# Kernel tuning notes

Hardware: AMD Instinct MI355X
Metric: run time of the kernel (lower is better)

## Reference

```python
import jax, jax.numpy as jnp
import numpy as np

MAX_FPS = 30.0
NUM_HEADS = 8


def _rope(x, times):
    # x: [B, H, T, D] with D even; interleaved rotary (even/odd pairs)
    B, H, T, D = x.shape
    inv_freq = 1.0 / (10000.0 ** (jnp.arange(0, D, 2, dtype=jnp.float32) / D))  # [D/2]
    pos = jnp.round(times * MAX_FPS)                       # [B, T]
    freqs = pos[:, :, None] * inv_freq[None, None, :]      # [B, T, D/2]
    cos = jnp.cos(freqs)[:, None, :, :]                    # [B, 1, T, D/2]
    sin = jnp.sin(freqs)[:, None, :, :]
    xp = x.reshape(B, H, T, D // 2, 2)
    x0, x1 = xp[..., 0], xp[..., 1]                        # even-index, odd-index elems
    r0 = x0 * cos - x1 * sin
    r1 = x0 * sin + x1 * cos
    return jnp.stack([r0, r1], axis=-1).reshape(B, H, T, D)


def setup_inputs() -> dict:
    key = jax.random.key(0)
    k1, k2, k3, k4, k5 = jax.random.split(key, 5)
    B, N, C = 4, 2048, 512
    x = jax.random.normal(k1, (B, N, C), dtype=jnp.float32)
    mask = jnp.zeros((B, N), dtype=jnp.float32)  # additive mask, 0 = attend
    # times in seconds; rounded to frame indices inside RoPE
    times = jax.random.uniform(k2, (B, N), dtype=jnp.float32) * (N / MAX_FPS)
    bound_qkv = float(np.sqrt(6.0 / (C + 3 * C)))
    Wqkv = jax.random.uniform(k3, (3 * C, C), minval=-bound_qkv, maxval=bound_qkv, dtype=jnp.float32)
    bound_p = float(np.sqrt(6.0 / (C + C)))
    Wproj = jax.random.uniform(k4, (C, C), minval=-bound_p, maxval=bound_p, dtype=jnp.float32)
    bproj = jnp.zeros((C,), dtype=jnp.float32)
    return {"x": x, "mask": mask, "times": times, "Wqkv": Wqkv,
            "Wproj": Wproj, "bproj": bproj, "num_cls_token": 0}


def reference(x, mask, times, Wqkv, Wproj, bproj, num_cls_token):
    B, N, C = x.shape
    H = NUM_HEADS
    Dh = C // H
    qkv = (x @ Wqkv.T).reshape(B, N, 3, H, Dh).transpose(2, 0, 3, 1, 4)  # [3,B,H,N,Dh]
    q, k, v = qkv[0], qkv[1], qkv[2]
    if num_cls_token > 0:
        c_q, q = q[:, :, :num_cls_token], q[:, :, num_cls_token:]
        c_k, k = k[:, :, :num_cls_token], k[:, :, num_cls_token:]
        t = times
        q = _rope(q, t)
        k = _rope(k, t)
        q = jnp.concatenate([c_q, q], axis=2)
        k = jnp.concatenate([c_k, k], axis=2)
    else:
        q = _rope(q, times)
        k = _rope(k, times)
    scale = 1.0 / jnp.sqrt(jnp.float32(Dh))
    scores = jnp.einsum('bhqd,bhkd->bhqk', q, k) * scale + mask[:, None, None, :]
    attn = jax.nn.softmax(scores, axis=-1)
    out = jnp.einsum('bhqk,bhkd->bhqd', attn, v)           # [B,H,N,Dh]
    out = out.transpose(0, 2, 1, 3).reshape(B, N, C)
    return out @ Wproj.T + bproj
```

## Files before the change

### kernel.cpp

```cpp
#include <hip/hip_runtime.h>
#include <math.h>

#define BB 4
#define NN 2048
#define CC 512
#define HH 8
#define DH 64
#define MM (BB*NN)
#define QKV_N (3*CC)
#define NSP 2
#define SLICE ((size_t)32 * NN)

typedef _Float16 f16;
typedef __attribute__((ext_vector_type(2))) _Float16 f16x2;
typedef __attribute__((ext_vector_type(4))) _Float16 f16x4;
typedef __attribute__((ext_vector_type(8))) _Float16 f16x8;
typedef __attribute__((ext_vector_type(4))) float f32x4;
typedef __attribute__((ext_vector_type(2))) __fp16 h16x2;

#define L2E 1.4426950408889634f
#define QSCL (0.125f * L2E)

__device__ __forceinline__ float fast_exp2(float x) {
#if __has_builtin(__builtin_amdgcn_exp2f)
    return __builtin_amdgcn_exp2f(x);
#else
    float r;
    asm volatile("v_exp_f32 %0, %1\n\ts_nop 1" : "=v"(r) : "v"(x));
    return r;
#endif
}

__device__ __forceinline__ float fdot2(f16x2 a, f16x2 b, float c) {
#if __has_builtin(__builtin_amdgcn_fdot2)
    return __builtin_amdgcn_fdot2(a, b, c, false);
#else
    return c + (float)a[0]*(float)b[0] + (float)a[1]*(float)b[1];
#endif
}

#define GL16(g, l) __builtin_amdgcn_global_load_lds(                       \
    (const __attribute__((address_space(1))) void*)(g),                    \
    (__attribute__((address_space(3))) void*)(l), 16, 0, 0)

#define SX4 (MM*CC/4)
#define SW4 (QKV_N*CC/4)
#define SP4 (CC*CC/4)
#define CAST_T (SX4 + SW4 + SP4)
#define TAB_T (MM * 32)
#define WT_T  (MM / 8)
__global__ __launch_bounds__(256) void cast_tab_kernel(
    const float* __restrict__ x, const float* __restrict__ wqkv,
    const float* __restrict__ wproj, const float* __restrict__ times,
    const float* __restrict__ mask,
    f16* __restrict__ xh, f16* __restrict__ wqh, f16* __restrict__ wph,
    float2* __restrict__ tab, f16* __restrict__ wtab)
{
    const int t = blockIdx.x * 256 + threadIdx.x;
    if (t < CAST_T) {
        const float* src; f16* dst; int i;
        bool qscale = false;
        if (t < SX4)            { src = x;     dst = xh;  i = t; }
        else if (t < SX4 + SW4) { src = wqkv;  dst = wqh; i = t - SX4;
                                  qscale = (i < CC*CC/4); }
        else                    { src = wproj; dst = wph; i = t - SX4 - SW4; }
        f32x4 v = *(const f32x4*)(src + 4 * (size_t)i);
        if (qscale) v *= QSCL;
        f16x4 h = { (f16)v[0], (f16)v[1], (f16)v[2], (f16)v[3] };
        *(f16x4*)(dst + 4 * (size_t)i) = h;
    } else if (t < CAST_T + TAB_T) {
        const int idx = t - CAST_T;
        const int row = idx >> 5, fi = idx & 31;
        const float pos = rintf(times[row] * 30.0f);
        const float invf = exp2f((float)fi * (-13.287712379549449f / 32.0f));
        float s, c;
        sincosf(pos * invf, &s, &c);
        tab[idx] = make_float2(c, s);
    } else {
        const int i = t - CAST_T - TAB_T;
        f32x4 m0 = *(const f32x4*)(mask + 8 * (size_t)i);
        f32x4 m1 = *(const f32x4*)(mask + 8 * (size_t)i + 4);
        f16x8 wv;
        #pragma unroll
        for (int r = 0; r < 4; ++r) {
            wv[r]     = (f16)fast_exp2(m0[r] * L2E);
            wv[4 + r] = (f16)fast_exp2(m1[r] * L2E);
        }
        *(f16x8*)(wtab + 8 * (size_t)i) = wv;
    }
}

__global__ __launch_bounds__(256) void qkv_gemm(
    const f16* __restrict__ xh, const f16* __restrict__ wh,
    const float2* __restrict__ tab, const int* __restrict__ nclsp,
    const f16* __restrict__ wtab,
    f16* __restrict__ qo, f16* __restrict__ ksw, f16* __restrict__ vsw)
{
    __shared__ __align__(16) char smem[16896];
    f16 (*As)[32] = (f16 (*)[32])smem;
    f16 (*Bs)[32] = (f16 (*)[32])(smem + 8192);

    const int m0 = blockIdx.x * 128;
    const int n0 = blockIdx.y * 128;
    const int tid = threadIdx.x;
    const int lane = tid & 63;
    const int w = tid >> 6;
    const int wm = (w & 1) * 64, wn = (w >> 1) * 64;
    const int l15 = lane & 15, quad = lane >> 4;

    const int sr = tid >> 2;
    const int sc = (tid & 3) * 8;
    const f16* ga0 = xh + (size_t)(m0 + sr) * CC + sc;
    const f16* ga1 = xh + (size_t)(m0 + sr + 64) * CC + sc;
    const f16* gb0 = wh + (size_t)(n0 + sr) * CC + sc;
    const f16* gb1 = wh + (size_t)(n0 + sr + 64) * CC + sc;
    f16* la0 = &As[sr][sc];      f16* la1 = &As[sr + 64][sc];
    f16* lb0 = &Bs[sr][sc];      f16* lb1 = &Bs[sr + 64][sc];

    f32x4 acc[4][4] = {};
    for (int k0 = 0; k0 < CC; k0 += 32) {
        __syncthreads();
        GL16(ga0 + k0, la0);
        GL16(ga1 + k0, la1);
        GL16(gb0 + k0, lb0);
        GL16(gb1 + k0, lb1);
        __syncthreads();

        f16x8 af[4], bf[4];
        #pragma unroll
        for (int mi = 0; mi < 4; ++mi)
            af[mi] = *(const f16x8*)&As[wm + mi*16 + l15][quad * 8];
        #pragma unroll
        for (int ni = 0; ni < 4; ++ni)
            bf[ni] = *(const f16x8*)&Bs[wn + ni*16 + l15][quad * 8];
        #pragma unroll
        for (int mi = 0; mi < 4; ++mi)
            #pragma unroll
            for (int ni = 0; ni < 4; ++ni)
                acc[mi][ni] = __builtin_amdgcn_mfma_f32_16x16x32_f16(
                    af[mi], bf[ni], acc[mi][ni], 0, 0, 0);
    }
    __syncthreads();

    const int which = n0 >> 9;
    const int b     = m0 >> 11;
    const int mloc  = m0 & (NN - 1);
    const int hbase = (n0 & 511) >> 6;

    if (which < 2) {
        f16 (*Tr)[132] = (f16 (*)[132])smem;
        const int ncls = *nclsp;
        #pragma unroll
        for (int c = 0; c < 2; ++c) {
            if ((w & 1) == c) {
                #pragma unroll
                for (int mi = 0; mi < 4; ++mi)
                    #pragma unroll
                    for (int ni = 0; ni < 4; ++ni)
                        #pragma unroll
                        for (int r = 0; r < 4; ++r)
                            Tr[16*mi + quad*4 + r][wn + 16*ni + l15] =
                                (f16)acc[mi][ni][r];
            }
            __syncthreads();
            const int row = tid >> 2, cg = tid & 3;
            const int n   = mloc + c*64 + row;
            const int hh  = hbase + (cg >> 1);
            const int d0  = (cg & 1) * 32;
            f16x8 vv[4];
            #pragma unroll
            for (int j = 0; j < 4; ++j)
                vv[j] = *(const f16x8*)&Tr[row][cg*32 + j*8];
            if (n >= ncls) {
                const f32x4* t4 = (const f32x4*)(tab + ((size_t)b*NN + n)*32
                                                 + (d0 >> 1));
                #pragma unroll
                for (int j = 0; j < 4; ++j) {
                    f32x4 cs0 = t4[2*j];
                    f32x4 cs1 = t4[2*j + 1];
                    #pragma unroll
                    for (int p = 0; p < 4; ++p) {
                        const float co = (p < 2) ? cs0[(p & 1)*2]
                                                 : cs1[(p & 1)*2];
                        const float s  = (p < 2) ? cs0[(p & 1)*2 + 1]
                                                 : cs1[(p & 1)*2 + 1];
                        const float x0 = (float)vv[j][2*p];
                        const float x1 = (float)vv[j][2*p+1];
                        vv[j][2*p]   = (f16)(x0*co - x1*s);
                        vv[j][2*p+1] = (f16)(x0*s + x1*co);
                    }
                }
            }
            if (which == 0) {
                f16* qp = qo + (((size_t)(b*HH + hh))*NN + n)*DH + d0;
                #pragma unroll
                for (int j = 0; j < 4; ++j)
                    *(f16x8*)(qp + 8*j) = vv[j];
            } else {
                const int ktile = (mloc >> 6) + c;
                f16* kp = ksw + ((((size_t)(b*HH + hh))*32 + ktile)*64 + row)*64;
                #pragma unroll
                for (int j = 0; j < 4; ++j) {
                    const int blk = (d0 >> 3) + j;
                    *(f16x8*)(kp + ((blk ^ (row & 7)) * 8)) = vv[j];
                }
            }
            if (c == 0) __syncthreads();
        }
        return;
    }

    f16 (*Tv)[66] = (f16 (*)[66])smem;
    #pragma unroll
    for (int c = 0; c < 2; ++c) {
        if ((w & 1) == c) {
            #pragma unroll
            for (int mi = 0; mi < 4; ++mi)
                #pragma unroll
                for (int ni = 0; ni < 4; ++ni) {
                    f16x4 pk = { (f16)acc[mi][ni][0], (f16)acc[mi][ni][1],
                                 (f16)acc[mi][ni][2], (f16)acc[mi][ni][3] };
                    *(f16x4*)&Tv[wn + 16*ni + l15][16*mi + quad*4] = pk;
                }
        }
        __syncthreads();
        const int rr = tid >> 1;
        const int d  = rr & 63, hh = hbase + (rr >> 6);
        const int ktile = (mloc >> 6) + c;
        f16* vp = vsw + ((((size_t)(b*HH + hh))*32 + ktile)*64 + d)*64;
        #pragma unroll
        for (int j = 0; j < 4; ++j) {
            const int blk = (tid & 1)*4 + j;
            f16x8 t = *(const f16x8*)&Tv[rr][(tid & 1)*32 + j*8];
            t *= *(const f16x8*)&wtab[(size_t)b*NN + mloc + c*64
                                      + (tid & 1)*32 + j*8];
            *(f16x8*)(vp + ((blk ^ (d & 7)) * 8)) = t;
        }
        if (c == 0) __syncthreads();
    }
}

__global__ __launch_bounds__(256, 4) void attn_kernel(
    const f16* __restrict__ qg, const f16* __restrict__ ksw,
    const f16* __restrict__ vsw, const f16* __restrict__ wtab,
    f16* __restrict__ On, float* __restrict__ lbuf)
{
    __shared__ __align__(16) f16 asm_[4][4096];

    const int bh = blockIdx.x, qt = blockIdx.y, sp = blockIdx.z;
    const int b = bh >> 3;
    const int tid = threadIdx.x;
    const int w = tid >> 6, lane = tid & 63;
    const int l15 = lane & 15, quad = lane >> 4;
    const int rho = l15 & 7;

    const f16* qbase = qg + ((size_t)bh * NN + qt*128 + w*32) * DH;
    const f16* kt0 = ksw + ((size_t)bh * 32 + sp*16) * 4096;
    const f16* vt0 = vsw + ((size_t)bh * 32 + sp*16) * 4096;
    const f16* wsl = wtab + (size_t)b * NN + sp*1024;

    f16x8 Bq[2][2];
    #pragma unroll
    for (int ni = 0; ni < 2; ++ni)
        #pragma unroll
        for (int kc = 0; kc < 2; ++kc)
            Bq[ni][kc] = *(const f16x8*)(qbase + (size_t)(16*ni + l15) * DH
                                         + kc*32 + quad*8);

    const f32x4 fz = {};
    f32x4 O[2][4] = {};
    float accL[2] = {};

    {
        const f16* ks = kt0 + tid*8;
        const f16* vs = vt0 + tid*8;
        GL16(ks,        &asm_[0][tid*8]);
        GL16(ks + 2048, &asm_[0][2048 + tid*8]);
        GL16(vs,        &asm_[1][tid*8]);
        GL16(vs + 2048, &asm_[1][2048 + tid*8]);
    }

    for (int kt = 0; kt < 16; ++kt) {
        const int cur = (kt & 1) * 2;
        __syncthreads();
        if (kt + 1 < 16) {
            const int nxt = 2 - cur;
            const f16* ks = kt0 + (size_t)(kt+1)*4096 + tid*8;
            const f16* vs = vt0 + (size_t)(kt+1)*4096 + tid*8;
            GL16(ks,        &asm_[nxt][tid*8]);
            GL16(ks + 2048, &asm_[nxt][2048 + tid*8]);
            GL16(vs,        &asm_[nxt+1][tid*8]);
            GL16(vs + 2048, &asm_[nxt+1][2048 + tid*8]);
        }
        const f16 (*Kh)[64] = (const f16 (*)[64])asm_[cur];
        const f16 (*Vt)[64] = (const f16 (*)[64])asm_[cur + 1];

        f32x4 st[4][2];
        const int aw = (quad ^ rho) * 8;
        __builtin_amdgcn_s_setprio(1);
        #pragma unroll
        for (int mi = 0; mi < 4; ++mi) {
            f16x8 Ak0 = *(const f16x8*)&Kh[16*mi + l15][aw];
            f16x8 Ak1 = *(const f16x8*)&Kh[16*mi + l15][aw ^ 32];
            #pragma unroll
            for (int ni = 0; ni < 2; ++ni) {
                f32x4 t0 = __builtin_amdgcn_mfma_f32_16x16x32_f16(
                    Ak0, Bq[ni][0], fz, 0, 0, 0);
                st[mi][ni] = __builtin_amdgcn_mfma_f32_16x16x32_f16(
                    Ak1, Bq[ni][1], t0, 0, 0, 0);
            }
        }
        __builtin_amdgcn_s_setprio(0);

        f16x4 ph[4][2];
        #pragma unroll
        for (int mi = 0; mi < 4; ++mi) {
            #pragma unroll
            for (int ni = 0; ni < 2; ++ni) {
                float e0 = fast_exp2(st[mi][ni][0]);
                float e1 = fast_exp2(st[mi][ni][1]);
                float e2 = fast_exp2(st[mi][ni][2]);
                float e3 = fast_exp2(st[mi][ni][3]);
                h16x2 lo = __builtin_amdgcn_cvt_pkrtz(e0, e1);
                h16x2 hi = __builtin_amdgcn_cvt_pkrtz(e2, e3);
                f16x2 lo2 = __builtin_bit_cast(f16x2, lo);
                f16x2 hi2 = __builtin_bit_cast(f16x2, hi);
                ph[mi][ni] = __builtin_shufflevector(lo2, hi2, 0, 1, 2, 3);
            }
            f16x4 wv = *(const f16x4*)(wsl + kt*64 + 16*mi + quad*4);
            f16x2 wlo = __builtin_shufflevector(wv, wv, 0, 1);
            f16x2 whi = __builtin_shufflevector(wv, wv, 2, 3);
            #pragma unroll
            for (int ni = 0; ni < 2; ++ni) {
                f16x2 plo = __builtin_shufflevector(ph[mi][ni], ph[mi][ni], 0, 1);
                f16x2 phi = __builtin_shufflevector(ph[mi][ni], ph[mi][ni], 2, 3);
                accL[ni] = fdot2(plo, wlo, accL[ni]);
                accL[ni] = fdot2(phi, whi, accL[ni]);
            }
        }

        __builtin_amdgcn_s_setprio(1);
        #pragma unroll
        for (int g = 0; g < 2; ++g) {
            f16x8 p0 = __builtin_shufflevector(ph[2*g][0], ph[2*g+1][0],
                                               0, 1, 2, 3, 4, 5, 6, 7);
            f16x8 p1 = __builtin_shufflevector(ph[2*g][1], ph[2*g+1][1],
                                               0, 1, 2, 3, 4, 5, 6, 7);
            const int vb1 = (((4*g + (quad >> 1)) ^ rho) * 8) + (quad & 1) * 4;
            const int vb2 = (((4*g + 2 + (quad >> 1)) ^ rho) * 8) + (quad & 1) * 4;
            #pragma unroll
            for (int nd = 0; nd < 4; ++nd) {
                f16x4 av0 = *(const f16x4*)&Vt[16*nd + l15][vb1];
                f16x4 av1 = *(const f16x4*)&Vt[16*nd + l15][vb2];
                f16x8 Av = __builtin_shufflevector(av0, av1,
                                                   0, 1, 2, 3, 4, 5, 6, 7);
                O[0][nd] = __builtin_amdgcn_mfma_f32_16x16x32_f16(
                    Av, p0, O[0][nd], 0, 0, 0);
                O[1][nd] = __builtin_amdgcn_mfma_f32_16x16x32_f16(
                    Av, p1, O[1][nd], 0, 0, 0);
            }
        }
        __builtin_amdgcn_s_setprio(0);
    }

    #pragma unroll
    for (int ni = 0; ni < 2; ++ni) {
        float l = accL[ni];
        l += __shfl_xor(l, 16);
        l += __shfl_xor(l, 32);
        const float inv = 1.0f / l;
        const int qrow = qt*128 + w*32 + 16*ni + l15;
        const size_t rbase = (size_t)sp * SLICE + (size_t)bh * NN + qrow;
        f16* obase = On + rbase * DH;
        #pragma unroll
        for (int nd = 0; nd < 4; ++nd) {
            f32x4 o = O[ni][nd] * inv;
            f16x4 oh = { (f16)o[0], (f16)o[1], (f16)o[2], (f16)o[3] };
            *(f16x4*)(obase + 16*nd + quad*4) = oh;
        }
        if (quad == 0)
            lbuf[rbase] = l;
    }
}

__global__ __launch_bounds__(256) void proj_gemm(
    const f16* __restrict__ On, const float* __restrict__ lbuf,
    const f16* __restrict__ wh, const float* __restrict__ bias,
    float* __restrict__ out)
{
    __shared__ f16 As[128][32];
    __shared__ f16 Bs[64][32];
    const int m0 = blockIdx.x * 128;
    const int n0 = blockIdx.y * 64;
    const int tid = threadIdx.x;
    const int lane = tid & 63;
    const int w = tid >> 6;
    const int wm = (w & 1) * 64, wn = (w >> 1) * 32;
    const int l15 = lane & 15, quad = lane >> 4;

    const int b  = m0 >> 11;
    const int q0 = m0 & (NN - 1);

    const int sr = tid >> 2;
    const int sc = (tid & 3) * 8;
    const f16* gb0 = wh + (size_t)(n0 + sr) * CC + sc;
    f16* lb0 = &Bs[sr][sc];

    f32x4 acc[4][2] = {};
    for (int k0 = 0; k0 < CC; k0 += 32) {
        const int h  = k0 >> 6;
        const int d0 = k0 & 63;
        __syncthreads();
        GL16(gb0 + k0, lb0);
        const size_t row0 = (size_t)(b*HH + h) * NN + q0 + sr;
        #pragma unroll
        for (int rr = 0; rr < 2; ++rr) {
            const size_t row = row0 + rr*64;
            const float l0 = lbuf[row], l1 = lbuf[SLICE + row];
            const float inv = 1.0f / (l0 + l1);
            const float w0 = l0 * inv, w1 = l1 * inv;
            f16x8 a0 = *(const f16x8*)(On + row * DH + d0 + sc);
            f16x8 a1 = *(const f16x8*)(On + (SLICE + row) * DH + d0 + sc);
            f16x8 o;
            #pragma unroll
            for (int r = 0; r < 8; ++r)
                o[r] = (f16)(w0 * (float)a0[r] + w1 * (float)a1[r]);
            *(f16x8*)&As[sr + rr*64][sc] = o;
        }
        __syncthreads();

        f16x8 af[4], bf[2];
        #pragma unroll
        for (int mi = 0; mi < 4; ++mi)
            af[mi] = *(const f16x8*)&As[wm + mi*16 + l15][quad * 8];
        #pragma unroll
        for (int ni = 0; ni < 2; ++ni)
            bf[ni] = *(const f16x8*)&Bs[wn + ni*16 + l15][quad * 8];
        #pragma unroll
        for (int mi = 0; mi < 4; ++mi)
            #pragma unroll
            for (int ni = 0; ni < 2; ++ni)
                acc[mi][ni] = __builtin_amdgcn_mfma_f32_16x16x32_f16(
                    af[mi], bf[ni], acc[mi][ni], 0, 0, 0);
    }

    float bb[2];
    #pragma unroll
    for (int ni = 0; ni < 2; ++ni)
        bb[ni] = bias[n0 + wn + ni*16 + l15];

    #pragma unroll
    for (int mi = 0; mi < 4; ++mi)
        #pragma unroll
        for (int r = 0; r < 4; ++r) {
            const int m = m0 + wm + mi*16 + quad*4 + r;
            #pragma unroll
            for (int ni = 0; ni < 2; ++ni)
                out[(size_t)m * CC + n0 + wn + ni*16 + l15] = acc[mi][ni][r] + bb[ni];
        }
}

extern "C" void kernel_launch(void* const* d_in, const int* in_sizes, int n_in,
                              void* d_out, int out_size, void* d_ws, size_t ws_size,
                              hipStream_t stream)
{
    const float* x     = (const float*)d_in[0];
    const float* mask  = (const float*)d_in[1];
    const float* times = (const float*)d_in[2];
    const float* Wqkv  = (const float*)d_in[3];
    const float* Wproj = (const float*)d_in[4];
    const float* bproj = (const float*)d_in[5];
    const int*   ncls  = (const int*)d_in[6];
    float* out = (float*)d_out;

    const size_t per = (size_t)BB * HH * NN * DH;
    f16* xh  = (f16*)d_ws;
    f16* wqh = xh + per;
    f16* wph = wqh + (size_t)QKV_N * CC;
    f16* q   = wph + (size_t)CC * CC;
    f16* ks  = q + per;
    f16* vs  = ks + per;
    f16* On  = vs + per;
    float* lb = (float*)(On + NSP * per);
    float2* tab = (float2*)(lb + NSP * 32 * NN);
    f16* wtab = (f16*)(tab + (size_t)MM * 32);

    cast_tab_kernel<<<(CAST_T + TAB_T + WT_T) / 256, 256, 0, stream>>>(
        x, Wqkv, Wproj, times, mask, xh, wqh, wph, tab, wtab);
    qkv_gemm<<<dim3(MM / 128, QKV_N / 128), 256, 0, stream>>>(
        xh, wqh, tab, ncls, wtab, q, ks, vs);
    attn_kernel<<<dim3(BB * HH, NN / 128, NSP), 256, 0, stream>>>(
        q, ks, vs, wtab, On, lb);
    proj_gemm<<<dim3(MM / 128, CC / 64), 256, 0, stream>>>(
        On, lb, wph, bproj, out);
}
```

Before: 171.6 us.

## Double-buffer shared-memory tiles in QKV and projection GEMMs

Both the QKV GEMM and the output projection GEMM now keep two shared-memory tile buffers per operand. The next K-slice is fetched while MFMAs run on the current one, which removes one barrier per iteration and hides global-load latency. In the projection GEMM, the split-attention operands and their row sums are prefetched into registers and combined one step later. This costs double the LDS per block, which may reduce occupancy, and adds register pressure.

```diff
diff --git a/kernel.cpp b/kernel.cpp
--- a/kernel.cpp
+++ b/kernel.cpp
@@ -96,9 +96,11 @@
     const f16* __restrict__ wtab,
     f16* __restrict__ qo, f16* __restrict__ ksw, f16* __restrict__ vsw)
 {
-    __shared__ __align__(16) char smem[16896];
-    f16 (*As)[32] = (f16 (*)[32])smem;
-    f16 (*Bs)[32] = (f16 (*)[32])(smem + 8192);
+    __shared__ __align__(16) char smem[32768];
+    f16 (*As0)[32] = (f16 (*)[32])smem;
+    f16 (*Bs0)[32] = (f16 (*)[32])(smem + 8192);
+    f16 (*As1)[32] = (f16 (*)[32])(smem + 16384);
+    f16 (*Bs1)[32] = (f16 (*)[32])(smem + 24576);
 
     const int m0 = blockIdx.x * 128;
     const int n0 = blockIdx.y * 128;
@@ -114,31 +116,41 @@
     const f16* ga1 = xh + (size_t)(m0 + sr + 64) * CC + sc;
     const f16* gb0 = wh + (size_t)(n0 + sr) * CC + sc;
     const f16* gb1 = wh + (size_t)(n0 + sr + 64) * CC + sc;
-    f16* la0 = &As[sr][sc];      f16* la1 = &As[sr + 64][sc];
-    f16* lb0 = &Bs[sr][sc];      f16* lb1 = &Bs[sr + 64][sc];
 
     f32x4 acc[4][4] = {};
-    for (int k0 = 0; k0 < CC; k0 += 32) {
+
+    GL16(ga0, &As0[sr][sc]);
+    GL16(ga1, &As0[sr + 64][sc]);
+    GL16(gb0, &Bs0[sr][sc]);
+    GL16(gb1, &Bs0[sr + 64][sc]);
+
+    auto step = [&](int k0, f16 (*Asc)[32], f16 (*Bsc)[32],
+                    f16 (*Asn)[32], f16 (*Bsn)[32]) {
         __syncthreads();
-        GL16(ga0 + k0, la0);
-        GL16(ga1 + k0, la1);
-        GL16(gb0 + k0, lb0);
-        GL16(gb1 + k0, lb1);
-        __syncthreads();
-
+        if (k0 + 32 < CC) {
+            GL16(ga0 + k0 + 32, &Asn[sr][sc]);
+            GL16(ga1 + k0 + 32, &Asn[sr + 64][sc]);
+            GL16(gb0 + k0 + 32, &Bsn[sr][sc]);
+            GL16(gb1 + k0 + 32, &Bsn[sr + 64][sc]);
+        }
         f16x8 af[4], bf[4];
         #pragma unroll
         for (int mi = 0; mi < 4; ++mi)
-            af[mi] = *(const f16x8*)&As[wm + mi*16 + l15][quad * 8];
+            af[mi] = *(const f16x8*)&Asc[wm + mi*16 + l15][quad * 8];
         #pragma unroll
         for (int ni = 0; ni < 4; ++ni)
-            bf[ni] = *(const f16x8*)&Bs[wn + ni*16 + l15][quad * 8];
+            bf[ni] = *(const f16x8*)&Bsc[wn + ni*16 + l15][quad * 8];
         #pragma unroll
         for (int mi = 0; mi < 4; ++mi)
             #pragma unroll
             for (int ni = 0; ni < 4; ++ni)
                 acc[mi][ni] = __builtin_amdgcn_mfma_f32_16x16x32_f16(
                     af[mi], bf[ni], acc[mi][ni], 0, 0, 0);
+    };
+    #pragma unroll
+    for (int kk = 0; kk < CC; kk += 64) {
+        step(kk,      As0, Bs0, As1, Bs1);
+        step(kk + 32, As1, Bs1, As0, Bs0);
     }
     __syncthreads();
 
@@ -388,8 +400,8 @@
     const f16* __restrict__ wh, const float* __restrict__ bias,
     float* __restrict__ out)
 {
-    __shared__ f16 As[128][32];
-    __shared__ f16 Bs[64][32];
+    __shared__ __align__(16) f16 As[2][128][32];
+    __shared__ __align__(16) f16 Bs[2][64][32];
     const int m0 = blockIdx.x * 128;
     const int n0 = blockIdx.y * 64;
     const int tid = threadIdx.x;
@@ -404,44 +416,62 @@
     const int sr = tid >> 2;
     const int sc = (tid & 3) * 8;
     const f16* gb0 = wh + (size_t)(n0 + sr) * CC + sc;
-    f16* lb0 = &Bs[sr][sc];
-
-    f32x4 acc[4][2] = {};
-    for (int k0 = 0; k0 < CC; k0 += 32) {
+
+    f16x8 pa0[2], pa1[2];
+    float pl0[2], pl1[2];
+    auto loadA = [&](int k0) {
         const int h  = k0 >> 6;
         const int d0 = k0 & 63;
-        __syncthreads();
-        GL16(gb0 + k0, lb0);
         const size_t row0 = (size_t)(b*HH + h) * NN + q0 + sr;
         #pragma unroll
         for (int rr = 0; rr < 2; ++rr) {
             const size_t row = row0 + rr*64;
-            const float l0 = lbuf[row], l1 = lbuf[SLICE + row];
-            const float inv = 1.0f / (l0 + l1);
-            const float w0 = l0 * inv, w1 = l1 * inv;
-            f16x8 a0 = *(const f16x8*)(On + row * DH + d0 + sc);
-            f16x8 a1 = *(const f16x8*)(On + (SLICE + row) * DH + d0 + sc);
+            pl0[rr] = lbuf[row];
+            pl1[rr] = lbuf[SLICE + row];
+            pa0[rr] = *(const f16x8*)(On + row * DH + d0 + sc);
+            pa1[rr] = *(const f16x8*)(On + (SLICE + row) * DH + d0 + sc);
+        }
+    };
+
+    f32x4 acc[4][2] = {};
+
+    auto step = [&](int k0, f16 (*Asc)[32], f16 (*Bsc)[32], f16 (*Bsn)[32]) {
+        #pragma unroll
+        for (int rr = 0; rr < 2; ++rr) {
+            const float inv = 1.0f / (pl0[rr] + pl1[rr]);
+            const float w0 = pl0[rr] * inv, w1 = pl1[rr] * inv;
             f16x8 o;
             #pragma unroll
             for (int r = 0; r < 8; ++r)
-                o[r] = (f16)(w0 * (float)a0[r] + w1 * (float)a1[r]);
-            *(f16x8*)&As[sr + rr*64][sc] = o;
+                o[r] = (f16)(w0 * (float)pa0[rr][r] + w1 * (float)pa1[rr][r]);
+            *(f16x8*)&Asc[sr + rr*64][sc] = o;
         }
         __syncthreads();
-
+        if (k0 + 32 < CC) {
+            GL16(gb0 + k0 + 32, &Bsn[sr][sc]);
+            loadA(k0 + 32);
+        }
         f16x8 af[4], bf[2];
         #pragma unroll
         for (int mi = 0; mi < 4; ++mi)
-            af[mi] = *(const f16x8*)&As[wm + mi*16 + l15][quad * 8];
+            af[mi] = *(const f16x8*)&Asc[wm + mi*16 + l15][quad * 8];
         #pragma unroll
         for (int ni = 0; ni < 2; ++ni)
-            bf[ni] = *(const f16x8*)&Bs[wn + ni*16 + l15][quad * 8];
+            bf[ni] = *(const f16x8*)&Bsc[wn + ni*16 + l15][quad * 8];
         #pragma unroll
         for (int mi = 0; mi < 4; ++mi)
             #pragma unroll
             for (int ni = 0; ni < 2; ++ni)
                 acc[mi][ni] = __builtin_amdgcn_mfma_f32_16x16x32_f16(
                     af[mi], bf[ni], acc[mi][ni], 0, 0, 0);
+    };
+
+    loadA(0);
+    GL16(gb0, &Bs[0][sr][sc]);
+    #pragma unroll
+    for (int kk = 0; kk < CC; kk += 64) {
+        step(kk,      As[0], Bs[0], Bs[1]);
+        step(kk + 32, As[1], Bs[1], Bs[0]);
     }
 
     float bb[2];
```

Measured after the change: 166.7 us. 2.8% less time.
